# Optimization experiments

Hardware: AMD Instinct MI355X
Metric: run time of the kernel (lower is better)

## Reference

```python
import jax, jax.numpy as jnp
import numpy as np

K = 3
OH = 62
OW = 62


def setup_inputs() -> dict:
    key = jax.random.key(0)
    k1, k2 = jax.random.split(key)
    x = jax.random.normal(k1, (32, 32, 64, 64), dtype=jnp.float32)
    W = jax.random.normal(k2, (64, 32, OH, OW, K, K), dtype=jnp.float32)
    b = jnp.zeros((64, OH, OW), dtype=jnp.float32)
    return {"x": x, "W": W, "b": b}


def _patches(x):
    # x: [B, C, H, W] -> [B, C, OH, OW, K, K] (stride-1 unfold, small K*K loop)
    return jnp.stack(
        [jnp.stack([x[:, :, i:i + OH, j:j + OW] for j in range(K)], axis=-1)
         for i in range(K)], axis=-2)


def reference(x, W, b):
    # Locally connected: per-location independent weights.
    # out[b,o,h,w] = sum_{c,i,j} x[b,c,h+i,w+j] * W[o,c,h,w,i,j] + b[o,h,w]
    p = _patches(x)  # [B, C, OH, OW, K, K]
    out = jnp.einsum('bchwij,ochwij->bohw', p, W) + b[None]
    return out
```

## Files before the change

### kernel.cpp

```cpp
#include <hip/hip_runtime.h>


#define C_  32
#define B_  32
#define O_  64
#define H_  64
#define W_  64
#define OH_ 62
#define OW_ 62

typedef float vfloat2 __attribute__((ext_vector_type(2)));
typedef float vfloat4 __attribute__((ext_vector_type(4)));

#define GLL4(gaddr, laddr)                                                      \
    __builtin_amdgcn_global_load_lds(                                           \
        (const __attribute__((address_space(1))) void*)(gaddr),                 \
        (__attribute__((address_space(3))) void*)(laddr), 4, 0, 0)

__device__ __forceinline__ float dpp_nextlane(float v) {
    return __int_as_float(__builtin_amdgcn_update_dpp(
        0, __float_as_int(v), 0x101, 0xf, 0xf, true));
}

#define WAITV(n) do {                                                           \
        asm volatile("s_waitcnt vmcnt(" #n ")" ::: "memory");                   \
        __builtin_amdgcn_sched_barrier(0);                                      \
    } while (0)

#define FENCE() __builtin_amdgcn_sched_barrier(0)

__global__ __launch_bounds__(256)
void lcl_kernel(const float* __restrict__ x,
                const float* __restrict__ Wt,
                const float* __restrict__ bias,
                float* __restrict__ out) {
    __shared__ float ldsW[2][4][2][576];

    const int i0      = blockIdx.x;
    const int logical = (i0 & 7) * 124 + (i0 >> 3);
    const int bhalf   = logical & 1;
    const int pair    = logical >> 1;
    const int og      = pair & 7;
    const int h       = pair >> 3;

    const int wv_i = threadIdx.x >> 6;
    const int o0   = (og << 3) + (wv_i << 1);
    const int lane = threadIdx.x & 63;
    const int wg   = lane & 15;
    const int bg   = lane >> 4;
    const int w0   = wg * 4;
    const int b0   = bhalf * 16 + bg * 4;
    const bool full = (wg < 15);

    float acc0[4][4], acc1[4][4];
#pragma unroll
    for (int bi = 0; bi < 4; ++bi)
#pragma unroll
        for (int wi = 0; wi < 4; ++wi) { acc0[bi][wi] = 0.f; acc1[bi][wi] = 0.f; }

    const long wrow0 = (long)o0 * (C_ * 34596) + (long)h * 558;
    const long wrow1 = wrow0 + (long)C_ * 34596;

    const char* xb0 = (const char*)x + (unsigned)b0 * 524288u
                      + (unsigned)h * 256u + (unsigned)wg * 16u;

#define STAGE_W2(buf, cidx) do {                                                \
        const char* s0_ = (const char*)(Wt + wrow0 + (long)(cidx) * 34596);     \
        const char* s1_ = (const char*)(Wt + wrow1 + (long)(cidx) * 34596);     \
        char* d0_ = (char*)&ldsW[buf][wv_i][0][0];                              \
        char* d1_ = (char*)&ldsW[buf][wv_i][1][0];                              \
        _Pragma("unroll")                                                       \
        for (int k_ = 0; k_ < 8; ++k_)                                          \
            GLL4(s0_ + k_ * 256 + lane * 4, d0_ + k_ * 256);                    \
        GLL4(s0_ + 1976 + lane * 4, d0_ + 1976);                                \
        _Pragma("unroll")                                                       \
        for (int k_ = 0; k_ < 8; ++k_)                                          \
            GLL4(s1_ + k_ * 256 + lane * 4, d1_ + k_ * 256);                    \
        GLL4(s1_ + 1976 + lane * 4, d1_ + 1976);                                \
    } while (0)

#define DSREAD_W(buf, oo_) do {                                                 \
        const char* r_ = (const char*)&ldsW[buf][wv_i][oo_][0] + wg * 144;      \
        _Pragma("unroll")                                                       \
        for (int q_ = 0; q_ < 9; ++q_)                                          \
            wq[q_] = *reinterpret_cast<const vfloat4*>(r_ + q_ * 16);           \
    } while (0)

#define WQ(t) (wq[(t) >> 2][(t) & 3])

#define XLD(s_, cidx, bi_) do {                                                 \
        const char* p_ = xb0 + (unsigned)(bi_) * 524288u                        \
                         + (unsigned)(cidx) * 16384u;                           \
        xv##s_[0] = *reinterpret_cast<const float4*>(p_);                       \
        xv##s_[1] = *reinterpret_cast<const float4*>(p_ + 256);                 \
        xv##s_[2] = *reinterpret_cast<const float4*>(p_ + 512);                 \
    } while (0)

#define FMA1(ACC, s_, bi_) do {                                                 \
        float xr_[3][6];                                                        \
        _Pragma("unroll")                                                       \
        for (int r_ = 0; r_ < 3; ++r_) {                                        \
            xr_[r_][0] = xv##s_[r_].x; xr_[r_][1] = xv##s_[r_].y;               \
            xr_[r_][2] = xv##s_[r_].z; xr_[r_][3] = xv##s_[r_].w;               \
            xr_[r_][4] = dpp_nextlane(xv##s_[r_].x);                            \
            xr_[r_][5] = dpp_nextlane(xv##s_[r_].y);                            \
        }                                                                       \
        _Pragma("unroll")                                                       \
        for (int wi_ = 0; wi_ < 4; ++wi_)                                       \
        _Pragma("unroll")                                                       \
        for (int ii_ = 0; ii_ < 3; ++ii_)                                       \
        _Pragma("unroll")                                                       \
        for (int j_ = 0; j_ < 3; ++j_)                                          \
            ACC[bi_][wi_] = fmaf(xr_[ii_][wi_ + j_],                            \
                                 WQ(wi_ * 9 + ii_ * 3 + j_), ACC[bi_][wi_]);    \
    } while (0)

    vfloat4 wq[9];
    float4  xvA[3], xvB[3], xvC[3], xvD[3];

    STAGE_W2(0, 0);
    STAGE_W2(1, 1);
    XLD(A, 0, 0);
    XLD(B, 0, 1);
    XLD(C, 0, 2);
    XLD(D, 0, 3);

    for (int c = 0; c < C_; ++c) {
        const int p = c & 1;
        WAITV(30);
        DSREAD_W(p, 0);
        FENCE();
        FMA1(acc0, A, 0);
        FMA1(acc0, B, 1);
        FMA1(acc0, C, 2);
        FMA1(acc0, D, 3);
        FENCE();
        DSREAD_W(p, 1);
        FENCE();
        FMA1(acc1, A, 0);
        FMA1(acc1, B, 1);
        FMA1(acc1, C, 2);
        FMA1(acc1, D, 3);
        FENCE();
        if (c + 1 < C_) {
            XLD(A, c + 1, 0);
            XLD(B, c + 1, 1);
            XLD(C, c + 1, 2);
            XLD(D, c + 1, 3);
        }
        FENCE();
        {
            const int cn = (c + 2 < C_) ? (c + 2) : (C_ - 1);
            STAGE_W2(p, cn);
        }
    }

#pragma unroll
    for (int oo = 0; oo < 2; ++oo) {
        const int oc = o0 + oo;
        const float* brow = bias + ((long)oc * OH_ + h) * OW_ + w0;
        float2 bv0 = *reinterpret_cast<const float2*>(brow);
        float2 bv1;
        if (full) bv1 = *reinterpret_cast<const float2*>(brow + 2);
        else { bv1.x = 0.f; bv1.y = 0.f; }
#pragma unroll
        for (int bi = 0; bi < 4; ++bi) {
            const float* a_ = oo ? acc1[bi] : acc0[bi];
            float* orow = out + (((long)(b0 + bi) * O_ + oc) * OH_ + h) * OW_ + w0;
            vfloat2 s0; s0.x = a_[0] + bv0.x; s0.y = a_[1] + bv0.y;
            __builtin_nontemporal_store(s0, reinterpret_cast<vfloat2*>(orow));
            if (full) {
                vfloat2 s1; s1.x = a_[2] + bv1.x; s1.y = a_[3] + bv1.y;
                __builtin_nontemporal_store(s1, reinterpret_cast<vfloat2*>(orow) + 1);
            }
        }
    }

#undef STAGE_W2
#undef DSREAD_W
#undef WQ
#undef XLD
#undef FMA1
}

extern "C" void kernel_launch(void* const* d_in, const int* in_sizes, int n_in,
                              void* d_out, int out_size, void* d_ws, size_t ws_size,
                              hipStream_t stream) {
    const float* x    = (const float*)d_in[0];
    const float* Wt   = (const float*)d_in[1];
    const float* bias = (const float*)d_in[2];
    float* out        = (float*)d_out;

    dim3 grid(992);
    dim3 block(256);
    lcl_kernel<<<grid, block, 0, stream>>>(x, Wt, bias, out);
}
```

Baseline: 140.1 us.

## Split channel reduction across two blocks with atomic accumulation

Splits the 32-channel reduction into two halves handled by separate blocks, doubling the grid from 992 to 1984 blocks. Partial sums are combined with float atomic adds into an output buffer zeroed by a new pre-pass kernel, and bias is added only by the first half. This aims to raise parallelism and occupancy across the CUs and cut per-block serial latency. In exchange it adds a zeroing launch, atomic traffic on the output, and a summation order that is no longer deterministic.

```diff
diff --git a/kernel.cpp b/kernel.cpp
--- a/kernel.cpp
+++ b/kernel.cpp
@@ -2,6 +2,7 @@
 
 
 #define C_  32
+#define CH_ 16
 #define B_  32
 #define O_  64
 #define H_  64
@@ -30,6 +31,14 @@
 #define FENCE() __builtin_amdgcn_sched_barrier(0)
 
 __global__ __launch_bounds__(256)
+void zero_kernel(float4* __restrict__ p, int n4) {
+    int i = blockIdx.x * blockDim.x + threadIdx.x;
+    const int stride = gridDim.x * blockDim.x;
+    float4 z; z.x = 0.f; z.y = 0.f; z.z = 0.f; z.w = 0.f;
+    for (; i < n4; i += stride) p[i] = z;
+}
+
+__global__ __launch_bounds__(256)
 void lcl_kernel(const float* __restrict__ x,
                 const float* __restrict__ Wt,
                 const float* __restrict__ bias,
@@ -37,11 +46,14 @@
     __shared__ float ldsW[2][4][2][576];
 
     const int i0      = blockIdx.x;
-    const int logical = (i0 & 7) * 124 + (i0 >> 3);
-    const int bhalf   = logical & 1;
-    const int pair    = logical >> 1;
+    const int logical = (i0 & 7) * 248 + (i0 >> 3);
+    const int chalf   = logical & 1;
+    const int l2      = logical >> 1;
+    const int bhalf   = l2 & 1;
+    const int pair    = l2 >> 1;
     const int og      = pair & 7;
     const int h       = pair >> 3;
+    const int c0      = chalf * CH_;
 
     const int wv_i = threadIdx.x >> 6;
     const int o0   = (og << 3) + (wv_i << 1);
@@ -58,10 +70,11 @@
 #pragma unroll
         for (int wi = 0; wi < 4; ++wi) { acc0[bi][wi] = 0.f; acc1[bi][wi] = 0.f; }
 
-    const long wrow0 = (long)o0 * (C_ * 34596) + (long)h * 558;
+    const long wrow0 = (long)o0 * (C_ * 34596) + (long)h * 558 + (long)c0 * 34596;
     const long wrow1 = wrow0 + (long)C_ * 34596;
 
     const char* xb0 = (const char*)x + (unsigned)b0 * 524288u
+                      + (unsigned)c0 * 16384u
                       + (unsigned)h * 256u + (unsigned)wg * 16u;
 
 #define STAGE_W2(buf, cidx) do {                                                \
@@ -125,7 +138,7 @@
     XLD(C, 0, 2);
     XLD(D, 0, 3);
 
-    for (int c = 0; c < C_; ++c) {
+    for (int c = 0; c < CH_; ++c) {
         const int p = c & 1;
         WAITV(30);
         DSREAD_W(p, 0);
@@ -142,7 +155,7 @@
         FMA1(acc1, C, 2);
         FMA1(acc1, D, 3);
         FENCE();
-        if (c + 1 < C_) {
+        if (c + 1 < CH_) {
             XLD(A, c + 1, 0);
             XLD(B, c + 1, 1);
             XLD(C, c + 1, 2);
@@ -150,7 +163,7 @@
         }
         FENCE();
         {
-            const int cn = (c + 2 < C_) ? (c + 2) : (C_ - 1);
+            const int cn = (c + 2 < CH_) ? (c + 2) : (CH_ - 1);
             STAGE_W2(p, cn);
         }
     }
@@ -158,21 +171,20 @@
 #pragma unroll
     for (int oo = 0; oo < 2; ++oo) {
         const int oc = o0 + oo;
-        const float* brow = bias + ((long)oc * OH_ + h) * OW_ + w0;
-        float2 bv0 = *reinterpret_cast<const float2*>(brow);
-        float2 bv1;
-        if (full) bv1 = *reinterpret_cast<const float2*>(brow + 2);
-        else { bv1.x = 0.f; bv1.y = 0.f; }
+        float bv[4] = {0.f, 0.f, 0.f, 0.f};
+        if (chalf == 0) {
+            const float* brow = bias + ((long)oc * OH_ + h) * OW_ + w0;
+            bv[0] = brow[0]; bv[1] = brow[1];
+            if (full) { bv[2] = brow[2]; bv[3] = brow[3]; }
+        }
+        const int nw = full ? 4 : 2;
 #pragma unroll
         for (int bi = 0; bi < 4; ++bi) {
             const float* a_ = oo ? acc1[bi] : acc0[bi];
             float* orow = out + (((long)(b0 + bi) * O_ + oc) * OH_ + h) * OW_ + w0;
-            vfloat2 s0; s0.x = a_[0] + bv0.x; s0.y = a_[1] + bv0.y;
-            __builtin_nontemporal_store(s0, reinterpret_cast<vfloat2*>(orow));
-            if (full) {
-                vfloat2 s1; s1.x = a_[2] + bv1.x; s1.y = a_[3] + bv1.y;
-                __builtin_nontemporal_store(s1, reinterpret_cast<vfloat2*>(orow) + 1);
-            }
+#pragma unroll
+            for (int wi = 0; wi < 4; ++wi)
+                if (wi < nw) unsafeAtomicAdd(orow + wi, a_[wi] + bv[wi]);
         }
     }
 
@@ -191,7 +203,9 @@
     const float* bias = (const float*)d_in[2];
     float* out        = (float*)d_out;
 
-    dim3 grid(992);
+    zero_kernel<<<2048, 256, 0, stream>>>((float4*)d_out, out_size / 4);
+
+    dim3 grid(1984);
     dim3 block(256);
     lcl_kernel<<<grid, block, 0, stream>>>(x, Wt, bias, out);
 }
```

Result: slower. 308.4 us (+120.1%).
